# Kernel tuning notes

Measured on AMD Instinct MI355X. Metric: run time of the kernel, lower is better.

Reference implementation:

```python
import jax, jax.numpy as jnp
import numpy as np

T, B, D, H = 256, 64, 512, 1024


def setup_inputs() -> dict:
    key = jax.random.key(0)
    ks = jax.random.split(key, 9)
    scale = 1.0 / np.sqrt(D + H)  # torch Linear default U(-1/sqrt(fan_in), 1/sqrt(fan_in))
    def lin(k):
        kw, kb = jax.random.split(k)
        W = jax.random.uniform(kw, (H, D + H), jnp.float32, -scale, scale)
        b = jax.random.uniform(kb, (H,), jnp.float32, -scale, scale)
        return W, b
    Wf, bf = lin(ks[0])
    Wi, bi = lin(ks[1])
    Wg, bg = lin(ks[2])
    Wo, bo = lin(ks[3])
    inputs = jax.random.normal(ks[4], (T, B, D), jnp.float32)
    return {"inputs": inputs, "Wf": Wf, "bf": bf, "Wi": Wi, "bi": bi,
            "Wg": Wg, "bg": bg, "Wo": Wo, "bo": bo}


def _lstm(inputs, Wf, bf, Wi, bi, Wg, bg, Wo, bo):
    # Stack the 4 gate linears into one GEMM: W_all [4H, D+H], b_all [4H]
    W_all = jnp.concatenate([Wf, Wi, Wg, Wo], axis=0)
    b_all = jnp.concatenate([bf, bi, bg, bo], axis=0)
    h0 = jnp.zeros((inputs.shape[1], Wf.shape[0]), inputs.dtype)
    c0 = jnp.zeros_like(h0)

    def step(carry, x):
        hx, cx = carry
        combined = jnp.concatenate([x, hx], axis=1)          # [B, D+H]
        gates = combined @ W_all.T + b_all                   # [B, 4H]
        f, i, g, o = jnp.split(gates, 4, axis=1)
        f = jax.nn.sigmoid(f)
        i = jax.nn.sigmoid(i)
        g = jnp.tanh(g)
        o = jax.nn.sigmoid(o)
        cx = f * cx + i * g
        hx = o * jnp.tanh(cx)
        return (hx, cx), hx

    (hT, cT), outputs = jax.lax.scan(step, (h0, c0), inputs)
    return outputs, (hT, cT)


def reference(inputs, Wf, bf, Wi, bi, Wg, bg, Wo, bo):
    return _lstm(inputs, Wf, bf, Wi, bi, Wg, bg, Wo, bo)
```

## Files before the change

kernel.cpp:

```cpp
#include <hip/hip_runtime.h>

#define T_STEPS 256
#define BATCH   64
#define DIN     512
#define HID     1024
#define KTOT    1536
#define NBLK    128
#define NPB     32
#define WPITCH  1544

#define OWNER(bl) ((((bl) & 7) << 4) | ((bl) >> 3))

typedef __attribute__((ext_vector_type(8))) short short8;
typedef __attribute__((ext_vector_type(4))) float f32x4;
typedef __attribute__((ext_vector_type(4))) int   i32x4;

#define WS_WPACK 0
#define WS_XBF   12648448
#define WS_HBF   29425664
#define WS_BPK   29687808
#define WS_SLOTS 29704192

#define MFMA(acc, a, b) acc = __builtin_amdgcn_mfma_f32_16x16x32_bf16(a, b, acc, 0, 0, 0)

#define GLD(D, P, OFF) \
  asm volatile("global_load_dwordx4 %0, %1, off offset:" #OFF " sc0 sc1" \
               : "=v"(D) : "v"(P))
#define TIE(N, x0, x1, x2, x3, x4, x5, x6, x7) \
  asm volatile("s_waitcnt vmcnt(" #N ")" \
               : "+v"(x0), "+v"(x1), "+v"(x2), "+v"(x3), \
                 "+v"(x4), "+v"(x5), "+v"(x6), "+v"(x7))

__device__ inline unsigned short f2bf(float x) {
  unsigned u = __builtin_bit_cast(unsigned, x);
  u += 0x7FFF + ((u >> 16) & 1);
  return (unsigned short)(u >> 16);
}

__global__ void prep_x(const float* __restrict__ x, ushort* __restrict__ Xbf,
                       ushort* __restrict__ hbf, unsigned* __restrict__ slots,
                       const float* __restrict__ bfv, const float* __restrict__ biv,
                       const float* __restrict__ bgv, const float* __restrict__ bov,
                       float* __restrict__ bpack) {
  unsigned i = blockIdx.x * 256 + threadIdx.x;
  float4 v = ((const float4*)x)[i];
  ushort4 o = make_ushort4(f2bf(v.x), f2bf(v.y), f2bf(v.z), f2bf(v.w));
  ((ushort4*)Xbf)[i] = o;
  if (i < (2 * BATCH * HID) / 4) ((ushort4*)hbf)[i] = make_ushort4(0, 0, 0, 0);
  if (i < NBLK * NPB) {
    int bl = i >> 5, n = i & 31, gate = n >> 3, jj = n & 7;
    int j = OWNER(bl) * 8 + jj;
    const float* b = (gate == 0) ? bfv : (gate == 1) ? biv : (gate == 2) ? bgv : bov;
    bpack[i] = b[j];
  }
  if (i < NBLK) slots[i] = 0;
}

__global__ void prep_w(const float* __restrict__ Wf, const float* __restrict__ Wi,
                       const float* __restrict__ Wg, const float* __restrict__ Wo,
                       ushort* __restrict__ Wpack) {
  int row = blockIdx.x;
  int bl = row >> 5, n = row & 31, gate = n >> 3, jj = n & 7;
  int j = OWNER(bl) * 8 + jj;
  const float* src = ((gate == 0) ? Wf : (gate == 1) ? Wi : (gate == 2) ? Wg : Wo)
                     + (size_t)j * KTOT;
  ushort* dst = Wpack + (size_t)row * WPITCH;
  for (int idx = threadIdx.x; idx < KTOT / 4; idx += 256) {
    float4 v = ((const float4*)src)[idx];
    ((ushort4*)dst)[idx] = make_ushort4(f2bf(v.x), f2bf(v.y), f2bf(v.z), f2bf(v.w));
  }
}

__launch_bounds__(256)
__global__ void lstm_persist(const ushort* __restrict__ Wpack,
                             const ushort* __restrict__ Xbf,
                             ushort* __restrict__ hbf,
                             const float* __restrict__ bpack,
                             unsigned* __restrict__ slots,
                             float* __restrict__ out) {
  __shared__ __align__(16) ushort Wlds[NPB * WPITCH];
  __shared__ float gates[NPB][BATCH + 4];
  __shared__ float blds[NPB];
  __shared__ float clds[8][BATCH + 1];

  const int tid  = threadIdx.x;
  const int bl   = blockIdx.x;
  const int lane = tid & 63;
  const int wave = tid >> 6;
  const int jbase = OWNER(bl) * 8;

  {
    const uint4* src = (const uint4*)(Wpack + (size_t)bl * NPB * WPITCH);
    uint4* dst = (uint4*)Wlds;
    for (int i = tid; i < NPB * WPITCH / 8; i += 256) dst[i] = src[i];
  }
  if (tid < NPB) blds[tid] = bpack[bl * NPB + tid];
  for (int i = tid; i < 8 * (BATCH + 1); i += 256) (&clds[0][0])[i] = 0.f;
  __syncthreads();

  const int m0    = wave * 16 + (lane & 15);
  const int kgrp8 = (lane >> 4) * 8;
  const ushort* wx0 = Wlds + (lane & 15) * WPITCH + kgrp8;
  const ushort* wx1 = wx0 + 16 * WPITCH;
  const ushort* wh0 = wx0 + DIN;
  const ushort* wh1 = wx1 + DIN;

  const f32x4 vzero = {0.f, 0.f, 0.f, 0.f};
  f32x4 acc00 = vzero, acc01 = vzero, acc10 = vzero, acc11 = vzero;

  auto xpart = [&](int t) {
    acc00 = vzero; acc01 = vzero; acc10 = vzero; acc11 = vzero;
    const ushort* xp = Xbf + ((size_t)t * BATCH + m0) * DIN + kgrp8;
#pragma unroll
    for (int ki = 0; ki < 16; ++ki) {
      short8 a  = *(const short8*)(xp + ki * 32);
      short8 b0 = *(const short8*)(wx0 + ki * 32);
      short8 b1 = *(const short8*)(wx1 + ki * 32);
      if (ki & 1) { MFMA(acc01, a, b0); MFMA(acc11, a, b1); }
      else        { MFMA(acc00, a, b0); MFMA(acc10, a, b1); }
    }
  };
  auto consume8 = [&](i32x4 v0, i32x4 v1, i32x4 v2, i32x4 v3,
                      i32x4 v4, i32x4 v5, i32x4 v6, i32x4 v7, int kiBase) {
    const ushort* b0p = wh0 + kiBase * 32;
    const ushort* b1p = wh1 + kiBase * 32;
    MFMA(acc00, __builtin_bit_cast(short8, v0), *(const short8*)(b0p + 0 * 32));
    MFMA(acc10, __builtin_bit_cast(short8, v0), *(const short8*)(b1p + 0 * 32));
    MFMA(acc01, __builtin_bit_cast(short8, v1), *(const short8*)(b0p + 1 * 32));
    MFMA(acc11, __builtin_bit_cast(short8, v1), *(const short8*)(b1p + 1 * 32));
    MFMA(acc00, __builtin_bit_cast(short8, v2), *(const short8*)(b0p + 2 * 32));
    MFMA(acc10, __builtin_bit_cast(short8, v2), *(const short8*)(b1p + 2 * 32));
    MFMA(acc01, __builtin_bit_cast(short8, v3), *(const short8*)(b0p + 3 * 32));
    MFMA(acc11, __builtin_bit_cast(short8, v3), *(const short8*)(b1p + 3 * 32));
    MFMA(acc00, __builtin_bit_cast(short8, v4), *(const short8*)(b0p + 4 * 32));
    MFMA(acc10, __builtin_bit_cast(short8, v4), *(const short8*)(b1p + 4 * 32));
    MFMA(acc01, __builtin_bit_cast(short8, v5), *(const short8*)(b0p + 5 * 32));
    MFMA(acc11, __builtin_bit_cast(short8, v5), *(const short8*)(b1p + 5 * 32));
    MFMA(acc00, __builtin_bit_cast(short8, v6), *(const short8*)(b0p + 6 * 32));
    MFMA(acc10, __builtin_bit_cast(short8, v6), *(const short8*)(b1p + 6 * 32));
    MFMA(acc01, __builtin_bit_cast(short8, v7), *(const short8*)(b0p + 7 * 32));
    MFMA(acc11, __builtin_bit_cast(short8, v7), *(const short8*)(b1p + 7 * 32));
  };

  xpart(0);
  for (int t = 0; t < T_STEPS; ++t) {
    if (tid < 64) {
      const unsigned tu = (unsigned)t;
      for (;;) {
        unsigned v0 = __hip_atomic_load(&slots[lane],      __ATOMIC_RELAXED, __HIP_MEMORY_SCOPE_AGENT);
        unsigned v1 = __hip_atomic_load(&slots[lane + 64], __ATOMIC_RELAXED, __HIP_MEMORY_SCOPE_AGENT);
        if (__all((v0 >= tu) && (v1 >= tu))) break;
        __builtin_amdgcn_s_sleep(1);
      }
    }
    __syncthreads();

    {
      const ushort* hb = hbf + (size_t)(t & 1) * (BATCH * HID)
                             + (size_t)m0 * HID + kgrp8;
      i32x4 p0, p1, p2, p3, p4, p5, p6, p7;
      i32x4 q0, q1, q2, q3, q4, q5, q6, q7;
      GLD(p0, hb, 0);    GLD(p1, hb, 64);   GLD(p2, hb, 128);  GLD(p3, hb, 192);
      GLD(p4, hb, 256);  GLD(p5, hb, 320);  GLD(p6, hb, 384);  GLD(p7, hb, 448);
      GLD(q0, hb, 512);  GLD(q1, hb, 576);  GLD(q2, hb, 640);  GLD(q3, hb, 704);
      GLD(q4, hb, 768);  GLD(q5, hb, 832);  GLD(q6, hb, 896);  GLD(q7, hb, 960);
      TIE(8, p0, p1, p2, p3, p4, p5, p6, p7);
      consume8(p0, p1, p2, p3, p4, p5, p6, p7, 0);
      GLD(p0, hb, 1024); GLD(p1, hb, 1088); GLD(p2, hb, 1152); GLD(p3, hb, 1216);
      GLD(p4, hb, 1280); GLD(p5, hb, 1344); GLD(p6, hb, 1408); GLD(p7, hb, 1472);
      TIE(8, q0, q1, q2, q3, q4, q5, q6, q7);
      consume8(q0, q1, q2, q3, q4, q5, q6, q7, 8);
      GLD(q0, hb, 1536); GLD(q1, hb, 1600); GLD(q2, hb, 1664); GLD(q3, hb, 1728);
      GLD(q4, hb, 1792); GLD(q5, hb, 1856); GLD(q6, hb, 1920); GLD(q7, hb, 1984);
      TIE(8, p0, p1, p2, p3, p4, p5, p6, p7);
      consume8(p0, p1, p2, p3, p4, p5, p6, p7, 16);
      TIE(0, q0, q1, q2, q3, q4, q5, q6, q7);
      consume8(q0, q1, q2, q3, q4, q5, q6, q7, 24);
    }

    {
      f32x4 g0 = acc00 + acc01, g1 = acc10 + acc11;
      int n0 = lane & 15;
      int mq = wave * 16 + (lane >> 4) * 4;
      *(f32x4*)&gates[n0][mq]      = g0;
      *(f32x4*)&gates[16 + n0][mq] = g1;
    }
    __syncthreads();

    if (tid < BATCH) {
      const int m = tid;
      float h8[8], c8[8];
#pragma unroll
      for (int jj = 0; jj < 8; ++jj) {
        float fp = gates[jj][m]      + blds[jj];
        float ip = gates[8 + jj][m]  + blds[8 + jj];
        float gp = gates[16 + jj][m] + blds[16 + jj];
        float op = gates[24 + jj][m] + blds[24 + jj];
        float fs = 1.f / (1.f + __expf(-fp));
        float is = 1.f / (1.f + __expf(-ip));
        float os = 1.f / (1.f + __expf(-op));
        float gt = 1.f - 2.f / (__expf(2.f * gp) + 1.f);
        float c  = fs * clds[jj][m] + is * gt;
        clds[jj][m] = c;
        float th = 1.f - 2.f / (__expf(2.f * c) + 1.f);
        h8[jj] = os * th;
        c8[jj] = c;
      }
      unsigned long long hl = (unsigned long long)f2bf(h8[0])
                            | ((unsigned long long)f2bf(h8[1]) << 16)
                            | ((unsigned long long)f2bf(h8[2]) << 32)
                            | ((unsigned long long)f2bf(h8[3]) << 48);
      unsigned long long hh = (unsigned long long)f2bf(h8[4])
                            | ((unsigned long long)f2bf(h8[5]) << 16)
                            | ((unsigned long long)f2bf(h8[6]) << 32)
                            | ((unsigned long long)f2bf(h8[7]) << 48);
      unsigned long long* hp64 =
          (unsigned long long*)(hbf + (size_t)((t + 1) & 1) * (BATCH * HID)
                                    + (size_t)m * HID + jbase);
      __hip_atomic_store(hp64,     hl, __ATOMIC_RELAXED, __HIP_MEMORY_SCOPE_AGENT);
      __hip_atomic_store(hp64 + 1, hh, __ATOMIC_RELAXED, __HIP_MEMORY_SCOPE_AGENT);
      asm volatile("s_waitcnt vmcnt(0)" ::: "memory");
      if (tid == 0)
        __hip_atomic_store(&slots[bl], (unsigned)(t + 1),
                           __ATOMIC_RELAXED, __HIP_MEMORY_SCOPE_AGENT);
      float* op0 = out + (size_t)t * (BATCH * HID) + (size_t)m * HID + jbase;
      *(float4*)op0       = make_float4(h8[0], h8[1], h8[2], h8[3]);
      *(float4*)(op0 + 4) = make_float4(h8[4], h8[5], h8[6], h8[7]);
      if (t == T_STEPS - 1) {
        float* hp = out + (size_t)T_STEPS * BATCH * HID + (size_t)m * HID + jbase;
        float* cp = hp + BATCH * HID;
        *(float4*)hp       = make_float4(h8[0], h8[1], h8[2], h8[3]);
        *(float4*)(hp + 4) = make_float4(h8[4], h8[5], h8[6], h8[7]);
        *(float4*)cp       = make_float4(c8[0], c8[1], c8[2], c8[3]);
        *(float4*)(cp + 4) = make_float4(c8[4], c8[5], c8[6], c8[7]);
      }
    }

    if (t < T_STEPS - 1) xpart(t + 1);
  }
}

extern "C" void kernel_launch(void* const* d_in, const int* in_sizes, int n_in,
                              void* d_out, int out_size, void* d_ws, size_t ws_size,
                              hipStream_t stream) {
  const float* x   = (const float*)d_in[0];
  const float* Wf  = (const float*)d_in[1];
  const float* bfv = (const float*)d_in[2];
  const float* Wi  = (const float*)d_in[3];
  const float* biv = (const float*)d_in[4];
  const float* Wg  = (const float*)d_in[5];
  const float* bgv = (const float*)d_in[6];
  const float* Wo  = (const float*)d_in[7];
  const float* bov = (const float*)d_in[8];

  char* ws = (char*)d_ws;
  ushort*   Wpack = (ushort*)(ws + WS_WPACK);
  ushort*   Xbf   = (ushort*)(ws + WS_XBF);
  ushort*   hbf   = (ushort*)(ws + WS_HBF);
  float*    bpack = (float*)(ws + WS_BPK);
  unsigned* slots = (unsigned*)(ws + WS_SLOTS);
  float*    out   = (float*)d_out;

  prep_x<<<dim3((T_STEPS * BATCH * DIN) / 4 / 256), dim3(256), 0, stream>>>(
      x, Xbf, hbf, slots, bfv, biv, bgv, bov, bpack);
  prep_w<<<dim3(NBLK * NPB), dim3(256), 0, stream>>>(Wf, Wi, Wg, Wo, Wpack);

  const ushort* Wpc = Wpack;
  const ushort* Xbc = Xbf;
  const float*  bpc = bpack;
  void* args[] = {(void*)&Wpc, (void*)&Xbc, (void*)&hbf,
                  (void*)&bpc, (void*)&slots, (void*)&out};
  hipLaunchCooperativeKernel((const void*)lstm_persist, dim3(NBLK), dim3(256),
                             args, 0, stream);
}
```

Measured before the change: 2.145 ms.

## Split per-step barrier into per-wave split polling and double-buffer gates LDS

Each wave now polls the readiness slots itself, in two halves: slots 0-63 before loading the first h chunk and slots 64-127 before the second. This replaces the single wave-0 poll followed by a block-wide barrier. The gates scratch buffer is double-buffered by step parity, so the barrier at the top of the step can go and the next step's writes cannot clash with the current step's reads. The block-to-hidden-column mapping becomes identity, which changes which slots cover which h columns. That only stays correct if the slot groups line up with the K chunks each load reads. The split overlaps waiting with loading, but adds polling traffic from every wave.

```diff
diff --git a/kernel.cpp b/kernel.cpp
--- a/kernel.cpp
+++ b/kernel.cpp
@@ -9,7 +9,7 @@
 #define NPB     32
 #define WPITCH  1544
 
-#define OWNER(bl) ((((bl) & 7) << 4) | ((bl) >> 3))
+#define OWNER(bl) (bl)
 
 typedef __attribute__((ext_vector_type(8))) short short8;
 typedef __attribute__((ext_vector_type(4))) float f32x4;
@@ -79,7 +79,7 @@
                              unsigned* __restrict__ slots,
                              float* __restrict__ out) {
   __shared__ __align__(16) ushort Wlds[NPB * WPITCH];
-  __shared__ float gates[NPB][BATCH + 4];
+  __shared__ float gates[2][NPB][BATCH + 4];
   __shared__ float blds[NPB];
   __shared__ float clds[8][BATCH + 1];
 
@@ -142,48 +142,49 @@
     MFMA(acc11, __builtin_bit_cast(short8, v7), *(const short8*)(b1p + 7 * 32));
   };
 
+  auto pollg = [&](int g, unsigned tu) {
+    const unsigned* sp = slots + (g << 6) + lane;
+    for (;;) {
+      unsigned v = __hip_atomic_load(sp, __ATOMIC_RELAXED, __HIP_MEMORY_SCOPE_AGENT);
+      if (__all(v >= tu)) break;
+      __builtin_amdgcn_s_sleep(1);
+    }
+    asm volatile("" ::: "memory");
+  };
+
   xpart(0);
   for (int t = 0; t < T_STEPS; ++t) {
-    if (tid < 64) {
-      const unsigned tu = (unsigned)t;
-      for (;;) {
-        unsigned v0 = __hip_atomic_load(&slots[lane],      __ATOMIC_RELAXED, __HIP_MEMORY_SCOPE_AGENT);
-        unsigned v1 = __hip_atomic_load(&slots[lane + 64], __ATOMIC_RELAXED, __HIP_MEMORY_SCOPE_AGENT);
-        if (__all((v0 >= tu) && (v1 >= tu))) break;
-        __builtin_amdgcn_s_sleep(1);
-      }
-    }
-    __syncthreads();
-
-    {
-      const ushort* hb = hbf + (size_t)(t & 1) * (BATCH * HID)
-                             + (size_t)m0 * HID + kgrp8;
-      i32x4 p0, p1, p2, p3, p4, p5, p6, p7;
-      i32x4 q0, q1, q2, q3, q4, q5, q6, q7;
-      GLD(p0, hb, 0);    GLD(p1, hb, 64);   GLD(p2, hb, 128);  GLD(p3, hb, 192);
-      GLD(p4, hb, 256);  GLD(p5, hb, 320);  GLD(p6, hb, 384);  GLD(p7, hb, 448);
-      GLD(q0, hb, 512);  GLD(q1, hb, 576);  GLD(q2, hb, 640);  GLD(q3, hb, 704);
-      GLD(q4, hb, 768);  GLD(q5, hb, 832);  GLD(q6, hb, 896);  GLD(q7, hb, 960);
-      TIE(8, p0, p1, p2, p3, p4, p5, p6, p7);
-      consume8(p0, p1, p2, p3, p4, p5, p6, p7, 0);
-      GLD(p0, hb, 1024); GLD(p1, hb, 1088); GLD(p2, hb, 1152); GLD(p3, hb, 1216);
-      GLD(p4, hb, 1280); GLD(p5, hb, 1344); GLD(p6, hb, 1408); GLD(p7, hb, 1472);
-      TIE(8, q0, q1, q2, q3, q4, q5, q6, q7);
-      consume8(q0, q1, q2, q3, q4, q5, q6, q7, 8);
-      GLD(q0, hb, 1536); GLD(q1, hb, 1600); GLD(q2, hb, 1664); GLD(q3, hb, 1728);
-      GLD(q4, hb, 1792); GLD(q5, hb, 1856); GLD(q6, hb, 1920); GLD(q7, hb, 1984);
-      TIE(8, p0, p1, p2, p3, p4, p5, p6, p7);
-      consume8(p0, p1, p2, p3, p4, p5, p6, p7, 16);
-      TIE(0, q0, q1, q2, q3, q4, q5, q6, q7);
-      consume8(q0, q1, q2, q3, q4, q5, q6, q7, 24);
-    }
+    const unsigned tu = (unsigned)t;
+    const ushort* hb = hbf + (size_t)(t & 1) * (BATCH * HID)
+                           + (size_t)m0 * HID + kgrp8;
+    i32x4 p0, p1, p2, p3, p4, p5, p6, p7;
+    i32x4 q0, q1, q2, q3, q4, q5, q6, q7;
+
+    pollg(0, tu);
+    GLD(p0, hb, 0);    GLD(p1, hb, 64);   GLD(p2, hb, 128);  GLD(p3, hb, 192);
+    GLD(p4, hb, 256);  GLD(p5, hb, 320);  GLD(p6, hb, 384);  GLD(p7, hb, 448);
+    pollg(1, tu);
+    GLD(q0, hb, 512);  GLD(q1, hb, 576);  GLD(q2, hb, 640);  GLD(q3, hb, 704);
+    GLD(q4, hb, 768);  GLD(q5, hb, 832);  GLD(q6, hb, 896);  GLD(q7, hb, 960);
+    TIE(8, p0, p1, p2, p3, p4, p5, p6, p7);
+    consume8(p0, p1, p2, p3, p4, p5, p6, p7, 0);
+    GLD(p0, hb, 1024); GLD(p1, hb, 1088); GLD(p2, hb, 1152); GLD(p3, hb, 1216);
+    GLD(p4, hb, 1280); GLD(p5, hb, 1344); GLD(p6, hb, 1408); GLD(p7, hb, 1472);
+    TIE(8, q0, q1, q2, q3, q4, q5, q6, q7);
+    consume8(q0, q1, q2, q3, q4, q5, q6, q7, 8);
+    GLD(q0, hb, 1536); GLD(q1, hb, 1600); GLD(q2, hb, 1664); GLD(q3, hb, 1728);
+    GLD(q4, hb, 1792); GLD(q5, hb, 1856); GLD(q6, hb, 1920); GLD(q7, hb, 1984);
+    TIE(8, p0, p1, p2, p3, p4, p5, p6, p7);
+    consume8(p0, p1, p2, p3, p4, p5, p6, p7, 16);
+    TIE(0, q0, q1, q2, q3, q4, q5, q6, q7);
+    consume8(q0, q1, q2, q3, q4, q5, q6, q7, 24);
 
     {
       f32x4 g0 = acc00 + acc01, g1 = acc10 + acc11;
       int n0 = lane & 15;
       int mq = wave * 16 + (lane >> 4) * 4;
-      *(f32x4*)&gates[n0][mq]      = g0;
-      *(f32x4*)&gates[16 + n0][mq] = g1;
+      *(f32x4*)&gates[t & 1][n0][mq]      = g0;
+      *(f32x4*)&gates[t & 1][16 + n0][mq] = g1;
     }
     __syncthreads();
 
@@ -192,10 +193,10 @@
       float h8[8], c8[8];
 #pragma unroll
       for (int jj = 0; jj < 8; ++jj) {
-        float fp = gates[jj][m]      + blds[jj];
-        float ip = gates[8 + jj][m]  + blds[8 + jj];
-        float gp = gates[16 + jj][m] + blds[16 + jj];
-        float op = gates[24 + jj][m] + blds[24 + jj];
+        float fp = gates[t & 1][jj][m]      + blds[jj];
+        float ip = gates[t & 1][8 + jj][m]  + blds[8 + jj];
+        float gp = gates[t & 1][16 + jj][m] + blds[16 + jj];
+        float op = gates[t & 1][24 + jj][m] + blds[24 + jj];
         float fs = 1.f / (1.f + __expf(-fp));
         float is = 1.f / (1.f + __expf(-ip));
         float os = 1.f / (1.f + __expf(-op));
```

After: 2.698 ms. +25.8%, slower.
